# Performance work log

Measured on AMD Instinct MI355X. Metric: run time of the kernel, lower is better.

Reference implementation:

```python
import jax, jax.numpy as jnp
import numpy as np


def setup_inputs() -> dict:
    key = jax.random.key(0)
    ks = jax.random.split(key, 6)
    B, C, H, W = 8, 256, 32, 32
    d = C // 8  # 32
    return {
        "x": jax.random.normal(ks[0], (B, C, H, W), dtype=jnp.float32),
        "Wq": jax.random.normal(ks[1], (d, C), dtype=jnp.float32) * 0.05,
        "bq": jnp.zeros((d,), dtype=jnp.float32),
        "Wk": jax.random.normal(ks[2], (d, C), dtype=jnp.float32) * 0.05,
        "bk": jnp.zeros((d,), dtype=jnp.float32),
        "Wv": jax.random.normal(ks[3], (C, C), dtype=jnp.float32) * 0.05,
        "bv": jnp.zeros((C,), dtype=jnp.float32),
        "Wr": jax.random.normal(ks[4], (d, 2), dtype=jnp.float32) * 0.05,
        "br": jnp.zeros((d,), dtype=jnp.float32),
        "gamma": jnp.array([0.5], dtype=jnp.float32),
    }


def reference(x, Wq, bq, Wk, bk, Wv, bv, Wr, br, gamma):
    B, C, H, W = x.shape
    N = H * W
    d = Wq.shape[0]
    xf = x.reshape(B, C, N)

    # 1x1 convs == per-pixel linear projections
    q = jnp.einsum('dc,bcn->bdn', Wq, xf) + bq[None, :, None]  # (B,d,N)
    k = jnp.einsum('dc,bcn->bdn', Wk, xf) + bk[None, :, None]  # (B,d,N)
    v = jnp.einsum('oc,bcn->bon', Wv, xf) + bv[None, :, None]  # (B,C,N)

    # relative position code: pairwise coord diffs through 1x1 conv (batch-independent)
    gh, gw = jnp.meshgrid(jnp.linspace(0.0, 1.0, H), jnp.linspace(0.0, 1.0, W), indexing='ij')
    coords = jnp.stack([gh.reshape(-1), gw.reshape(-1)])  # (2,N)
    diff = coords[:, :, None] - coords[:, None, :]         # (2,N,N)
    rp_code = jnp.einsum('dt,tij->dij', Wr, diff) + br[:, None, None]  # (d,N,N)

    scale = 1.0 / jnp.sqrt(jnp.asarray(d, dtype=x.dtype))
    score = jnp.einsum('bdi,bdj->bij', q, k) * scale          # (B,N,N)
    rp_score = jnp.einsum('bdi,dij->bij', q, rp_code) * scale  # (B,N,N)
    attn = jax.nn.softmax(score + rp_score, axis=-1)

    # out[b,c,i] = sum_j v[b,c,j] * attn[b,i,j]
    out = jnp.einsum('bcj,bij->bci', v, attn)
    return gamma[0] * out.reshape(B, C, H, W) + x
```

## Files before the change

### kernel.cpp

```cpp
#include <hip/hip_runtime.h>
#include <hip/hip_bf16.h>

#define BATCH 8
#define CH    256
#define NN    1024
#define DD    32

#define QT_OFF 0
#define KT_OFF (BATCH * NN * DD)
#define V_OFF  (2 * BATCH * NN * DD)
#define V2_B   (NN * CH)

#define SCALE 0.17677669529663687f
#define INV31 (1.0f / 31.0f)

typedef __attribute__((ext_vector_type(4))) float f32x4;
typedef __attribute__((ext_vector_type(8))) short bf16x8;

__device__ __forceinline__ unsigned int packbf2(float lo, float hi) {
    __hip_bfloat162 h = __float22bfloat162_rn(make_float2(lo, hi));
    union { __hip_bfloat162 h; unsigned int u; } cv; cv.h = h;
    return cv.u;
}
__device__ __forceinline__ unsigned short f2bf(float x) {
    union { float f; unsigned int u; } v; v.f = x;
    return (unsigned short)((v.u + 0x7FFFu + ((v.u >> 16) & 1u)) >> 16);
}

__global__ __launch_bounds__(256) void proj_kernel(
    const float* __restrict__ x,
    const float* __restrict__ Wq, const float* __restrict__ bq,
    const float* __restrict__ Wk, const float* __restrict__ bk,
    const float* __restrict__ Wv, const float* __restrict__ bv,
    const float* __restrict__ Wr,
    unsigned short* __restrict__ ws)
{
    const int nt   = blockIdx.x;
    const int b    = blockIdx.y;
    const int tid  = threadIdx.x;
    const int wv   = tid >> 6;
    const int lane = tid & 63;
    const int n16  = lane & 15;
    const int q4   = lane >> 4;
    const int n    = nt * 16 + n16;

    f32x4 acc[5];
#pragma unroll
    for (int t = 0; t < 5; t++) acc[t] = (f32x4){0.f, 0.f, 0.f, 0.f};

    const float* wrow[5];
#pragma unroll
    for (int t = 0; t < 5; t++) {
        const int m = (wv * 5 + t) * 16 + n16;
        wrow[t] = (m < 32) ? (Wq + m * CH)
                : (m < 64) ? (Wk + (m - 32) * CH)
                           : (Wv + (m - 64) * CH);
    }

    for (int c0 = 0; c0 < CH; c0 += 32) {
        const int kofs = c0 + q4 * 8;
        float bx[8];
#pragma unroll
        for (int jj = 0; jj < 8; jj++)
            bx[jj] = x[(size_t)(b * CH + kofs + jj) * NN + n];
        union { unsigned int u[4]; bf16x8 v; } bf;
#pragma unroll
        for (int p = 0; p < 4; p++) bf.u[p] = packbf2(bx[2 * p], bx[2 * p + 1]);

#pragma unroll
        for (int t = 0; t < 5; t++) {
            const float* wp = wrow[t] + kofs;
            const float4 a0 = *(const float4*)(wp);
            const float4 a1 = *(const float4*)(wp + 4);
            union { unsigned int u[4]; bf16x8 v; } af;
            af.u[0] = packbf2(a0.x, a0.y); af.u[1] = packbf2(a0.z, a0.w);
            af.u[2] = packbf2(a1.x, a1.y); af.u[3] = packbf2(a1.z, a1.w);
            acc[t] = __builtin_amdgcn_mfma_f32_16x16x32_bf16(af.v, bf.v, acc[t], 0, 0, 0);
        }
    }

    const int jt  = n >> 5;
    const int q4p = (n >> 3) & 3;
    const int jj  = n & 7;
#pragma unroll
    for (int t = 0; t < 5; t++) {
        const int mf = wv * 5 + t;
        const int mb = mf * 16 + q4 * 4;
        if (mb < 32) {
            const float r0 = (acc[t][0] + bq[mb + 0]) * SCALE;
            const float r1 = (acc[t][1] + bq[mb + 1]) * SCALE;
            const float r2 = (acc[t][2] + bq[mb + 2]) * SCALE;
            const float r3 = (acc[t][3] + bq[mb + 3]) * SCALE;
            uint2 st = { packbf2(r0, r1), packbf2(r2, r3) };
            *(uint2*)(ws + QT_OFF + (size_t)(b * NN + n) * DD + mb) = st;
        } else if (mb < 64) {
            const int d = mb - 32;
            const float An = (float)(n >> 5) * INV31;
            const float Bn = (float)(n & 31) * INV31;
            float r[4];
#pragma unroll
            for (int rr = 0; rr < 4; rr++)
                r[rr] = acc[t][rr] + bk[d + rr] - An * Wr[2 * (d + rr)] - Bn * Wr[2 * (d + rr) + 1];
            uint2 st = { packbf2(r[0], r[1]), packbf2(r[2], r[3]) };
            *(uint2*)(ws + KT_OFF + (size_t)(b * NN + n) * DD + d) = st;
        } else {
            const int c = mb - 64;
#pragma unroll
            for (int rr = 0; rr < 4; rr++) {
                const int cc = c + rr;
                const size_t off = V_OFF + (size_t)b * V2_B
                                 + (size_t)jt * 8192 + (size_t)(cc >> 4) * 512
                                 + (size_t)(q4p * 16 + (cc & 15)) * 8 + jj;
                ws[off] = f2bf(acc[t][rr] + bv[cc]);
            }
        }
    }
}

__global__ __launch_bounds__(512) void attn_kernel(
    const float* __restrict__ x,
    const float* __restrict__ gamma,
    const unsigned short* __restrict__ ws,
    float* __restrict__ out)
{
    const int it   = blockIdx.x;
    const int b    = blockIdx.y;
    const int tid  = threadIdx.x;
    const int wv   = (tid >> 6) & 3;
    const int jh   = tid >> 8;
    const int lane = tid & 63;
    const int n    = lane & 15;
    const int q4   = lane >> 4;
    const int i0   = it * 16;
    const int cb   = wv * 64;

    __shared__ float accL[4 * 16 * 64];
    __shared__ float lL[16];

    const unsigned short* qT = ws + QT_OFF + (size_t)b * NN * DD;
    const unsigned short* kT = ws + KT_OFF + (size_t)b * NN * DD + (size_t)jh * 512 * DD;
    const unsigned short* vb = ws + V_OFF + (size_t)b * V2_B
                             + (size_t)jh * 16 * 8192 + (size_t)wv * 4 * 512
                             + (size_t)lane * 8;

    const bf16x8 qf = *(const bf16x8*)(qT + (size_t)(i0 + n) * DD + q4 * 8);

    f32x4 acc[4];
#pragma unroll
    for (int t = 0; t < 4; t++) acc[t] = (f32x4){0.f, 0.f, 0.f, 0.f};
    float lsum = 0.f;

    bf16x8 ka0 = *(const bf16x8*)(kT + (size_t)(n) * DD + q4 * 8);
    bf16x8 ka1 = *(const bf16x8*)(kT + (size_t)(16 + n) * DD + q4 * 8);
    bf16x8 va[4];
#pragma unroll
    for (int t = 0; t < 4; t++)
        va[t] = *(const bf16x8*)(vb + t * 512);

    const int qh2 = (q4 & 1) * 2;

#pragma unroll 4
    for (int ch = 0; ch < 16; ch++) {
        const bf16x8 ka0c = ka0, ka1c = ka1;
        bf16x8 vac[4];
#pragma unroll
        for (int t = 0; t < 4; t++) vac[t] = va[t];

        {
            const int j0 = (ch + 1) * 32;
            ka0 = *(const bf16x8*)(kT + (size_t)(j0 + n) * DD + q4 * 8);
            ka1 = *(const bf16x8*)(kT + (size_t)(j0 + 16 + n) * DD + q4 * 8);
#pragma unroll
            for (int t = 0; t < 4; t++)
                va[t] = *(const bf16x8*)(vb + (ch + 1) * 8192 + t * 512);
        }

        const f32x4 z = {0.f, 0.f, 0.f, 0.f};
        f32x4 s0 = __builtin_amdgcn_mfma_f32_16x16x32_bf16(ka0c, qf, z, 0, 0, 0);
        f32x4 s1 = __builtin_amdgcn_mfma_f32_16x16x32_bf16(ka1c, qf, z, 0, 0, 0);

        float p0[4], p1[4];
#pragma unroll
        for (int r = 0; r < 4; r++) {
            p0[r] = __expf(s0[r]);
            p1[r] = __expf(s1[r]);
            lsum += p0[r] + p1[r];
        }

        unsigned int pk0[2] = { packbf2(p0[0], p0[1]), packbf2(p0[2], p0[3]) };
        unsigned int pk1[2] = { packbf2(p1[0], p1[1]), packbf2(p1[2], p1[3]) };
        union { unsigned int u[4]; bf16x8 v; } pf;
#pragma unroll
        for (int t = 0; t < 4; t++) {
            const int src = (qh2 + (t >> 1)) * 16 + n;
            const unsigned int lo = (unsigned int)__shfl((int)pk0[t & 1], src, 64);
            const unsigned int hi = (unsigned int)__shfl((int)pk1[t & 1], src, 64);
            pf.u[t] = (q4 >= 2) ? hi : lo;
        }

#pragma unroll
        for (int t = 0; t < 4; t++)
            acc[t] = __builtin_amdgcn_mfma_f32_16x16x32_bf16(vac[t], pf.v, acc[t], 0, 0, 0);
    }

    lsum += __shfl_xor(lsum, 16, 64);
    lsum += __shfl_xor(lsum, 32, 64);

    if (jh == 1) {
#pragma unroll
        for (int t = 0; t < 4; t++)
#pragma unroll
            for (int r = 0; r < 4; r++)
                accL[(wv * 16 + t * 4 + r) * 64 + lane] = acc[t][r];
        if (wv == 0 && lane < 16) lL[lane] = lsum;
    }
    __syncthreads();

    if (jh == 0) {
        const float ltot = lsum + lL[n];
        const float rl = gamma[0] / ltot;
#pragma unroll
        for (int t = 0; t < 4; t++) {
#pragma unroll
            for (int r = 0; r < 4; r++) {
                const float a = acc[t][r] + accL[(wv * 16 + t * 4 + r) * 64 + lane];
                const int c = cb + t * 16 + q4 * 4 + r;
                const size_t idx = (size_t)(b * CH + c) * NN + i0 + n;
                out[idx] = a * rl + x[idx];
            }
        }
    }
}

extern "C" void kernel_launch(void* const* d_in, const int* in_sizes, int n_in,
                              void* d_out, int out_size, void* d_ws, size_t ws_size,
                              hipStream_t stream) {
    (void)in_sizes; (void)n_in; (void)out_size; (void)ws_size;
    const float* x     = (const float*)d_in[0];
    const float* Wq    = (const float*)d_in[1];
    const float* bq    = (const float*)d_in[2];
    const float* Wk    = (const float*)d_in[3];
    const float* bk    = (const float*)d_in[4];
    const float* Wv    = (const float*)d_in[5];
    const float* bv    = (const float*)d_in[6];
    const float* Wr    = (const float*)d_in[7];
    const float* gamma = (const float*)d_in[9];
    float* out = (float*)d_out;
    unsigned short* ws = (unsigned short*)d_ws;

    proj_kernel<<<dim3(64, 8), 256, 0, stream>>>(x, Wq, bq, Wk, bk, Wv, bv, Wr, ws);
    attn_kernel<<<dim3(64, 8), 512, 0, stream>>>(x, gamma, ws, out);
}
```

Baseline: 119.5 us.

## Prepack weights to bf16, double-buffer projection loads, split attention blocks by channel

Adds a small kernel that converts the Q/K/V weights to bf16 once per call, stored in the MFMA fragment layout. The projection kernel can then load ready-made fragments and double-buffer both the x and weight loads across the K loop. The attention kernel is split into 256-thread blocks that each cover half the channels, which doubles the block count, and the grid is reordered so the batch index is on the x dimension. The log2(e) factor is folded into the Q scale so exp2f can replace __expf. The cost is a third kernel launch and QK/softmax work that is now done twice, once in each channel-half block.

```diff
diff --git a/kernel.cpp b/kernel.cpp
--- a/kernel.cpp
+++ b/kernel.cpp
@@ -10,8 +10,9 @@
 #define KT_OFF (BATCH * NN * DD)
 #define V_OFF  (2 * BATCH * NN * DD)
 #define V2_B   (NN * CH)
-
-#define SCALE 0.17677669529663687f
+#define WF_OFF (V_OFF + BATCH * V2_B)
+
+#define SCALE_Q (0.17677669529663687f * 1.4426950408889634f)
 #define INV31 (1.0f / 31.0f)
 
 typedef __attribute__((ext_vector_type(4))) float f32x4;
@@ -27,12 +28,29 @@
     return (unsigned short)((v.u + 0x7FFFu + ((v.u >> 16) & 1u)) >> 16);
 }
 
-__global__ __launch_bounds__(256) void proj_kernel(
+__global__ __launch_bounds__(256) void wrepack_kernel(
+    const float* __restrict__ Wq, const float* __restrict__ Wk,
+    const float* __restrict__ Wv, unsigned short* __restrict__ ws)
+{
+    const int gid = blockIdx.x * 256 + threadIdx.x;
+    const int e = gid * 4;
+    const int m = e >> 8;
+    const int k = e & 255;
+    const float* src = (m < 32) ? (Wq + m * CH + k)
+                     : (m < 64) ? (Wk + (m - 32) * CH + k)
+                                : (Wv + (m - 64) * CH + k);
+    const float4 w = *(const float4*)src;
+    const int mf = m >> 4, kc = k >> 5;
+    const int lf = ((k >> 3) & 3) * 16 + (m & 15);
+    const int jj = k & 7;
+    uint2 st = { packbf2(w.x, w.y), packbf2(w.z, w.w) };
+    *(uint2*)(ws + WF_OFF + ((size_t)(mf * 8 + kc) * 64 + lf) * 8 + jj) = st;
+}
+
+__global__ __launch_bounds__(256, 2) void proj_kernel(
     const float* __restrict__ x,
-    const float* __restrict__ Wq, const float* __restrict__ bq,
-    const float* __restrict__ Wk, const float* __restrict__ bk,
-    const float* __restrict__ Wv, const float* __restrict__ bv,
-    const float* __restrict__ Wr,
+    const float* __restrict__ bq, const float* __restrict__ bk,
+    const float* __restrict__ bv, const float* __restrict__ Wr,
     unsigned short* __restrict__ ws)
 {
     const int nt   = blockIdx.x;
@@ -48,35 +66,36 @@
 #pragma unroll
     for (int t = 0; t < 5; t++) acc[t] = (f32x4){0.f, 0.f, 0.f, 0.f};
 
-    const float* wrow[5];
-#pragma unroll
-    for (int t = 0; t < 5; t++) {
-        const int m = (wv * 5 + t) * 16 + n16;
-        wrow[t] = (m < 32) ? (Wq + m * CH)
-                : (m < 64) ? (Wk + (m - 32) * CH)
-                           : (Wv + (m - 64) * CH);
-    }
-
-    for (int c0 = 0; c0 < CH; c0 += 32) {
-        const int kofs = c0 + q4 * 8;
-        float bx[8];
-#pragma unroll
-        for (int jj = 0; jj < 8; jj++)
-            bx[jj] = x[(size_t)(b * CH + kofs + jj) * NN + n];
+    const unsigned short* wfl = ws + WF_OFF + (size_t)lane * 8;
+    const float* xb = x + (size_t)b * CH * NN + n;
+
+    float  bx[2][8];
+    bf16x8 af[2][5];
+#pragma unroll
+    for (int jj = 0; jj < 8; jj++)
+        bx[0][jj] = xb[(size_t)(q4 * 8 + jj) * NN];
+#pragma unroll
+    for (int t = 0; t < 5; t++)
+        af[0][t] = *(const bf16x8*)(wfl + (size_t)((wv * 5 + t) * 8) * 512);
+
+#pragma unroll
+    for (int kc = 0; kc < 8; kc++) {
+        const int s = kc & 1;
+        if (kc < 7) {
+            const int kofs = (kc + 1) * 32 + q4 * 8;
+#pragma unroll
+            for (int jj = 0; jj < 8; jj++)
+                bx[s ^ 1][jj] = xb[(size_t)(kofs + jj) * NN];
+#pragma unroll
+            for (int t = 0; t < 5; t++)
+                af[s ^ 1][t] = *(const bf16x8*)(wfl + (size_t)((wv * 5 + t) * 8 + kc + 1) * 512);
+        }
         union { unsigned int u[4]; bf16x8 v; } bf;
 #pragma unroll
-        for (int p = 0; p < 4; p++) bf.u[p] = packbf2(bx[2 * p], bx[2 * p + 1]);
-
-#pragma unroll
-        for (int t = 0; t < 5; t++) {
-            const float* wp = wrow[t] + kofs;
-            const float4 a0 = *(const float4*)(wp);
-            const float4 a1 = *(const float4*)(wp + 4);
-            union { unsigned int u[4]; bf16x8 v; } af;
-            af.u[0] = packbf2(a0.x, a0.y); af.u[1] = packbf2(a0.z, a0.w);
-            af.u[2] = packbf2(a1.x, a1.y); af.u[3] = packbf2(a1.z, a1.w);
-            acc[t] = __builtin_amdgcn_mfma_f32_16x16x32_bf16(af.v, bf.v, acc[t], 0, 0, 0);
-        }
+        for (int p = 0; p < 4; p++) bf.u[p] = packbf2(bx[s][2 * p], bx[s][2 * p + 1]);
+#pragma unroll
+        for (int t = 0; t < 5; t++)
+            acc[t] = __builtin_amdgcn_mfma_f32_16x16x32_bf16(af[s][t], bf.v, acc[t], 0, 0, 0);
     }
 
     const int jt  = n >> 5;
@@ -87,10 +106,10 @@
         const int mf = wv * 5 + t;
         const int mb = mf * 16 + q4 * 4;
         if (mb < 32) {
-            const float r0 = (acc[t][0] + bq[mb + 0]) * SCALE;
-            const float r1 = (acc[t][1] + bq[mb + 1]) * SCALE;
-            const float r2 = (acc[t][2] + bq[mb + 2]) * SCALE;
-            const float r3 = (acc[t][3] + bq[mb + 3]) * SCALE;
+            const float r0 = (acc[t][0] + bq[mb + 0]) * SCALE_Q;
+            const float r1 = (acc[t][1] + bq[mb + 1]) * SCALE_Q;
+            const float r2 = (acc[t][2] + bq[mb + 2]) * SCALE_Q;
+            const float r3 = (acc[t][3] + bq[mb + 3]) * SCALE_Q;
             uint2 st = { packbf2(r0, r1), packbf2(r2, r3) };
             *(uint2*)(ws + QT_OFF + (size_t)(b * NN + n) * DD + mb) = st;
         } else if (mb < 64) {
@@ -117,30 +136,32 @@
     }
 }
 
-__global__ __launch_bounds__(512) void attn_kernel(
+__global__ __launch_bounds__(256, 4) void attn_kernel(
     const float* __restrict__ x,
     const float* __restrict__ gamma,
     const unsigned short* __restrict__ ws,
     float* __restrict__ out)
 {
-    const int it   = blockIdx.x;
-    const int b    = blockIdx.y;
+    const int b    = blockIdx.x;
+    const int by   = blockIdx.y;
+    const int ig   = by >> 1;
+    const int cs   = by & 1;
     const int tid  = threadIdx.x;
-    const int wv   = (tid >> 6) & 3;
-    const int jh   = tid >> 8;
+    const int jh   = tid >> 7;
+    const int cw   = (tid >> 6) & 1;
     const int lane = tid & 63;
     const int n    = lane & 15;
     const int q4   = lane >> 4;
-    const int i0   = it * 16;
-    const int cb   = wv * 64;
-
-    __shared__ float accL[4 * 16 * 64];
+    const int i0   = ig * 16;
+    const int cb   = cs * 128 + cw * 64;
+
+    __shared__ float accL[2 * 16 * 64];
     __shared__ float lL[16];
 
     const unsigned short* qT = ws + QT_OFF + (size_t)b * NN * DD;
     const unsigned short* kT = ws + KT_OFF + (size_t)b * NN * DD + (size_t)jh * 512 * DD;
     const unsigned short* vb = ws + V_OFF + (size_t)b * V2_B
-                             + (size_t)jh * 16 * 8192 + (size_t)wv * 4 * 512
+                             + (size_t)jh * 16 * 8192 + (size_t)(cb >> 4) * 512
                              + (size_t)lane * 8;
 
     const bf16x8 qf = *(const bf16x8*)(qT + (size_t)(i0 + n) * DD + q4 * 8);
@@ -158,6 +179,9 @@
         va[t] = *(const bf16x8*)(vb + t * 512);
 
     const int qh2 = (q4 & 1) * 2;
+    int src[4];
+#pragma unroll
+    for (int t = 0; t < 4; t++) src[t] = (qh2 + (t >> 1)) * 16 + n;
 
 #pragma unroll 4
     for (int ch = 0; ch < 16; ch++) {
@@ -182,8 +206,8 @@
         float p0[4], p1[4];
 #pragma unroll
         for (int r = 0; r < 4; r++) {
-            p0[r] = __expf(s0[r]);
-            p1[r] = __expf(s1[r]);
+            p0[r] = exp2f(s0[r]);
+            p1[r] = exp2f(s1[r]);
             lsum += p0[r] + p1[r];
         }
 
@@ -192,9 +216,8 @@
         union { unsigned int u[4]; bf16x8 v; } pf;
 #pragma unroll
         for (int t = 0; t < 4; t++) {
-            const int src = (qh2 + (t >> 1)) * 16 + n;
-            const unsigned int lo = (unsigned int)__shfl((int)pk0[t & 1], src, 64);
-            const unsigned int hi = (unsigned int)__shfl((int)pk1[t & 1], src, 64);
+            const unsigned int lo = (unsigned int)__shfl((int)pk0[t & 1], src[t], 64);
+            const unsigned int hi = (unsigned int)__shfl((int)pk1[t & 1], src[t], 64);
             pf.u[t] = (q4 >= 2) ? hi : lo;
         }
 
@@ -211,21 +234,20 @@
         for (int t = 0; t < 4; t++)
 #pragma unroll
             for (int r = 0; r < 4; r++)
-                accL[(wv * 16 + t * 4 + r) * 64 + lane] = acc[t][r];
-        if (wv == 0 && lane < 16) lL[lane] = lsum;
+                accL[(cw * 16 + t * 4 + r) * 64 + lane] = acc[t][r];
+        if (cw == 0 && lane < 16) lL[lane] = lsum;
     }
     __syncthreads();
 
     if (jh == 0) {
-        const float ltot = lsum + lL[n];
-        const float rl = gamma[0] / ltot;
+        const float rl = gamma[0] / (lsum + lL[n]);
 #pragma unroll
         for (int t = 0; t < 4; t++) {
 #pragma unroll
             for (int r = 0; r < 4; r++) {
-                const float a = acc[t][r] + accL[(wv * 16 + t * 4 + r) * 64 + lane];
                 const int c = cb + t * 16 + q4 * 4 + r;
                 const size_t idx = (size_t)(b * CH + c) * NN + i0 + n;
+                const float a = acc[t][r] + accL[(cw * 16 + t * 4 + r) * 64 + lane];
                 out[idx] = a * rl + x[idx];
             }
         }
@@ -248,6 +270,7 @@
     float* out = (float*)d_out;
     unsigned short* ws = (unsigned short*)d_ws;
 
-    proj_kernel<<<dim3(64, 8), 256, 0, stream>>>(x, Wq, bq, Wk, bk, Wv, bv, Wr, ws);
-    attn_kernel<<<dim3(64, 8), 512, 0, stream>>>(x, gamma, ws, out);
-}
+    wrepack_kernel<<<80, 256, 0, stream>>>(Wq, Wk, Wv, ws);
+    proj_kernel<<<dim3(64, 8), 256, 0, stream>>>(x, bq, bk, bv, Wr, ws);
+    attn_kernel<<<dim3(8, 128), 256, 0, stream>>>(x, gamma, ws, out);
+}
```

After: 108.0 us (median of 2 runs). 1.11x faster.
